# Kernel tuning notes

Hardware: AMD Instinct MI355X
Metric: run time of the kernel (lower is better)

## Reference

```python
import jax, jax.numpy as jnp
import numpy as np

S, H, D, NL = 3, 64, 12, 2  # scales, hidden, input_dim, layers
B, L = 512, 512
EPS = 1e-5


def _layernorm(x, g, b):
    m = jnp.mean(x, axis=-1, keepdims=True)
    v = jnp.var(x, axis=-1, keepdims=True)
    return (x - m) * jax.lax.rsqrt(v + EPS) * g + b


def _cell(x_t, h, c, gw, gb, mi_w, mi_b, mo_w, mo_b, w1, b1, w2, b2, lag, lab, log, lob):
    # fused 4-gate linear: [B, in+H] @ [in+H, 4H]
    gates = jnp.concatenate([x_t, h], axis=-1) @ gw + gb
    f, i, g, o = jnp.split(gates, 4, axis=-1)
    c_new = jax.nn.sigmoid(f) * c + jax.nn.sigmoid(i) * jnp.tanh(g)
    h_t = jax.nn.sigmoid(o) * jnp.tanh(c_new)
    # MultiheadAttention with seq_len=1: softmax over one key == 1,
    # so attn_out = out_proj(v_proj(h_t)) exactly (q/k contribute nothing).
    v = h_t @ mi_w[:, 2 * H:] + mi_b[2 * H:]
    a = v @ mo_w + mo_b
    a = jax.nn.gelu(a @ w1 + b1, approximate=False) @ w2 + b2
    a = _layernorm(a, lag, lab)
    return _layernorm(a + h, log, lob), c_new


def _run_xlstm(xi, gw0, gb0, gw1, gb1, mi_w, mi_b, mo_w, mo_b,
               w1, b1, w2, b2, lag, lab, log, lob, rw0, rb0, rw1, rb1):
    # xi: [B, L, D] -> outputs [B, L, H]; 2-layer unidirectional xLSTM (eval: dropout=identity)
    Bb = xi.shape[0]
    z = jnp.zeros((Bb, H), xi.dtype)

    def step(carry, x_t):
        h0, c0, h1, c1 = carry
        h0, c0 = _cell(x_t, h0, c0, gw0, gb0, mi_w[0], mi_b[0], mo_w[0], mo_b[0],
                       w1[0], b1[0], w2[0], b2[0], lag[0], lab[0], log[0], lob[0])
        inp = h0 + x_t @ rw0 + rb0
        h1, c1 = _cell(inp, h1, c1, gw1, gb1, mi_w[1], mi_b[1], mo_w[1], mo_b[1],
                       w1[1], b1[1], w2[1], b2[1], lag[1], lab[1], log[1], lob[1])
        out = h1 + inp @ rw1 + rb1
        return (h0, c0, h1, c1), out

    _, ys = jax.lax.scan(step, (z, z, z, z), jnp.swapaxes(xi, 0, 1))
    return jnp.swapaxes(ys, 0, 1)


def _upsample_linear(xi, out_len):
    # F.interpolate(mode='linear', align_corners=False) on [B, Li, D] time axis
    Li = xi.shape[1]
    if Li == out_len:
        return xi
    sc = Li / out_len
    src = jnp.maximum((jnp.arange(out_len, dtype=jnp.float32) + 0.5) * sc - 0.5, 0.0)
    i0 = jnp.clip(jnp.floor(src).astype(jnp.int32), 0, Li - 1)
    i1 = jnp.minimum(i0 + 1, Li - 1)
    w = (src - i0.astype(jnp.float32))[None, :, None]
    return xi[:, i0] * (1.0 - w) + xi[:, i1] * w


def _forward(x, gw0, gb0, gw1, gb1, mi_w, mi_b, mo_w, mo_b, w1, b1, w2, b2,
             lag, lab, log, lob, rw0, rb0, rw1, rb1, attn_w):
    Ls = x.shape[1]
    ups = []
    for i in (1, 2, 3):
        start = Ls - Ls // i
        ups.append(_upsample_linear(x[:, start:, :], Ls))
    # bug-faithful ordering from source: xlstm[i] consumes upsampled_outputs[i-1]
    xs = jnp.stack([ups[2], ups[0], ups[1]], axis=0)  # [S, B, L, D]
    outs = jax.vmap(_run_xlstm)(xs, gw0, gb0, gw1, gb1, mi_w, mi_b, mo_w, mo_b,
                                w1, b1, w2, b2, lag, lab, log, lob,
                                rw0, rb0, rw1, rb1)      # [S, B, L, H]
    merged = jnp.moveaxis(outs, 0, 1)                    # [B, S, L, H]
    weights = jax.nn.softmax(merged @ attn_w, axis=1)    # softmax over scale dim
    return jnp.sum(merged * weights[..., None], axis=1)  # [B, L, H]


def setup_inputs() -> dict:
    key = jax.random.key(0)
    ks = iter(jax.random.split(key, 32))
    w = lambda *sh: jax.random.normal(next(ks), sh, jnp.float32) * 0.02
    IN0, IN1 = D + H, 2 * H
    return {
        'x': jax.random.normal(next(ks), (B, L, D), jnp.float32),
        'gw0': w(S, IN0, 4 * H), 'gb0': jnp.zeros((S, 4 * H)),
        'gw1': w(S, IN1, 4 * H), 'gb1': jnp.zeros((S, 4 * H)),
        'mi_w': w(S, NL, H, 3 * H), 'mi_b': jnp.zeros((S, NL, 3 * H)),
        'mo_w': w(S, NL, H, H), 'mo_b': jnp.zeros((S, NL, H)),
        'w1': w(S, NL, H, 2 * H), 'b1': jnp.zeros((S, NL, 2 * H)),
        'w2': w(S, NL, 2 * H, H), 'b2': jnp.zeros((S, NL, H)),
        'lag': jnp.ones((S, NL, H)), 'lab': jnp.zeros((S, NL, H)),
        'log': jnp.ones((S, NL, H)), 'lob': jnp.zeros((S, NL, H)),
        'rw0': w(S, D, H), 'rb0': jnp.zeros((S, H)),
        'rw1': w(S, H, H), 'rb1': jnp.zeros((S, H)),
        'attn_w': w(H),
    }


def reference(x, gw0, gb0, gw1, gb1, mi_w, mi_b, mo_w, mo_b, w1, b1, w2, b2,
              lag, lab, log, lob, rw0, rb0, rw1, rb1, attn_w):
    return _forward(x, gw0, gb0, gw1, gb1, mi_w, mi_b, mo_w, mo_b, w1, b1, w2, b2,
                    lag, lab, log, lob, rw0, rb0, rw1, rb1, attn_w)
```

## Files before the change

kernel.cpp:

```cpp
#include <hip/hip_runtime.h>
#include <hip/hip_bf16.h>
#include <math.h>

#define Sn 3
#define Hn 64
#define Dn 12
#define Bn 512
#define Ln 512
#define BC 4
#define IN0 76
#define NIN 22
#define CT 32
#define NCHUNK (Ln / CT)
#define P2OFF 0
#define P1OFF 384
#define GROFF 768
#define CBOFF 1026
#define MEGABLK 1538

#define NINP ((size_t)3 * Bn * CT * 64)
#define NG1R ((size_t)3 * Bn * CT * 320)
#define NMERG ((size_t)3 * Bn * CT * 64)

using bf16 = __hip_bfloat16;
typedef _Float16 h2 __attribute__((ext_vector_type(2)));
typedef _Float16 h4 __attribute__((ext_vector_type(4)));
typedef _Float16 h8t __attribute__((ext_vector_type(8)));
typedef int i2v __attribute__((ext_vector_type(2)));

__device__ __forceinline__ float u2f(unsigned short x) {
    return __uint_as_float(((unsigned int)x) << 16);
}
__device__ __forceinline__ unsigned short f2u(float f) {
    bf16 h = __float2bfloat16(f);
    unsigned short u;
    __builtin_memcpy(&u, &h, 2);
    return u;
}

__device__ __forceinline__ float ex2(float x) {
#if __has_builtin(__builtin_amdgcn_exp2f)
    return __builtin_amdgcn_exp2f(x);
#else
    return exp2f(x);
#endif
}
__device__ __forceinline__ float frcp(float x) {
#if __has_builtin(__builtin_amdgcn_rcpf)
    return __builtin_amdgcn_rcpf(x);
#else
    return 1.0f / x;
#endif
}
__device__ __forceinline__ float sigm(float x) {
    return frcp(1.0f + ex2(-1.44269504f * x));
}
__device__ __forceinline__ float tanhfast(float x) {
    return 1.0f - 2.0f * frcp(1.0f + ex2(2.88539008f * x));
}
__device__ __forceinline__ float gelu_ex(float x) { return 0.5f * x * (1.0f + erff(x * 0.70710678118654752f)); }

__device__ __forceinline__ float fdot2f(h2 a, h2 b, float c) {
#if __has_builtin(__builtin_amdgcn_fdot2)
    return __builtin_amdgcn_fdot2(a, b, c, false);
#else
    return fmaf((float)a.x, (float)b.x, fmaf((float)a.y, (float)b.y, c));
#endif
}
__device__ __forceinline__ h2 cvt2(float x, float y) {
    h2 r; r.x = (_Float16)x; r.y = (_Float16)y; return r;
}
__device__ __forceinline__ h2 mk2(_Float16 a, _Float16 b) {
    h2 r; r.x = a; r.y = b; return r;
}
__device__ __forceinline__ void unpack8(h8t v, h2* out) {
    out[0] = __builtin_shufflevector(v, v, 0, 1);
    out[1] = __builtin_shufflevector(v, v, 2, 3);
    out[2] = __builtin_shufflevector(v, v, 4, 5);
    out[3] = __builtin_shufflevector(v, v, 6, 7);
}

template <int CTRL>
__device__ __forceinline__ float qp(float v) {
    return __int_as_float(__builtin_amdgcn_update_dpp(0, __float_as_int(v), CTRL, 0xF, 0xF, true));
}
__device__ __forceinline__ float qsum(float v) {
    v += qp<0xB1>(v);
    v += qp<0x4E>(v);
    return v;
}
__device__ __forceinline__ float osum(float v) {
    v = qsum(v);
    v += qp<0x141>(v);
    return v;
}
__device__ __forceinline__ float xadd16(float v) {
#if __has_builtin(__builtin_amdgcn_permlane16_swap)
    i2v r = __builtin_amdgcn_permlane16_swap(__float_as_int(v), __float_as_int(v), false, false);
    return __int_as_float(r.x) + __int_as_float(r.y);
#else
    return v + __int_as_float(__builtin_amdgcn_ds_swizzle(__float_as_int(v), 0x401F));
// ... 40 lines not shown
    unsigned dstOff[NIN];
    unsigned n[NIN];
    unsigned blockStart[NIN + 1];
};

__global__ __launch_bounds__(256) void convert_kernel(ConvArgs a, float* __restrict__ dst,
                                                      const int* __restrict__ flag) {
    int bid = blockIdx.x;
    int i = 0;
    while (i < NIN - 1 && bid >= (int)a.blockStart[i + 1]) i++;
    unsigned lb = (unsigned)bid - a.blockStart[i];
    unsigned base = lb * 2048 + threadIdx.x;
    unsigned n = a.n[i];
    float* d = dst + a.dstOff[i];
    bool isf32 = (*flag != 0);
    const float* sf = (const float*)a.src[i];
    const unsigned short* su = (const unsigned short*)a.src[i];
#pragma unroll
    for (int e = 0; e < 8; e++) {
        unsigned idx = base + e * 256;
        if (idx < n) d[idx] = isf32 ? sf[idx] : u2f(su[idx]);
    }
}

__global__ __launch_bounds__(256) void fuse_kernel(
    const float* __restrict__ mi_w, const float* __restrict__ mi_b,
    const float* __restrict__ mo_w, const float* __restrict__ mo_b,
    const float* __restrict__ w1, const float* __restrict__ b1,
    float* __restrict__ M1out, float* __restrict__ bias1out) {
    int sl = blockIdx.x;
    __shared__ float T[64][64];
    __shared__ float bT[64];
    const float* Mv = mi_w + sl * 64 * 192;
    const float* Mo = mo_w + sl * 64 * 64;
    for (int idx = threadIdx.x; idx < 64 * 64; idx += 256) {
        int k = idx >> 6, n = idx & 63;
        float acc = 0.f;
        for (int j = 0; j < 64; j++) acc += Mv[k * 192 + 128 + j] * Mo[j * 64 + n];
        T[k][n] = acc;
    }
    for (int n = threadIdx.x; n < 64; n += 256) {
        float acc = mo_b[sl * 64 + n];
        for (int j = 0; j < 64; j++) acc += mi_b[sl * 192 + 128 + j] * Mo[j * 64 + n];
        bT[n] = acc;
    }
    __syncthreads();
    const float* W1 = w1 + sl * 64 * 128;
    for (int idx = threadIdx.x; idx < 64 * 128; idx += 256) {
        int k = idx >> 7, m = idx & 127;
        float acc = 0.f;
        for (int n = 0; n < 64; n++) acc += T[k][n] * W1[n * 128 + m];
        M1out[sl * 64 * 128 + idx] = acc;
    }
    for (int m = threadIdx.x; m < 128; m += 256) {
        float acc = b1[sl * 128 + m];
        for (int n = 0; n < 64; n++) acc += bT[n] * W1[n * 128 + m];
        bias1out[sl * 128 + m] = acc;
    }
}

__global__ __launch_bounds__(256) void perm_kernel(
    const float* __restrict__ gw1, const float* __restrict__ gb1,
    const float* __restrict__ rw1,
    h2* __restrict__ gw1p16, float* __restrict__ gb1p,
    h2* __restrict__ rw1p16) {
    int s = blockIdx.x;
    int tid = threadIdx.x;
    const float* G = gw1 + (size_t)s * 128 * 256;
    for (int idx = tid; idx < 32 * 256; idx += 256) {
        int k2 = idx >> 8, p = idx & 255;
        int c = (p & 3) * 64 + ((p >> 6) << 4) + ((p >> 2) & 15);
        gw1p16[((size_t)s * 32 + k2) * 256 + p] =
            cvt2(G[(2 * k2) * 256 + c], G[(2 * k2 + 1) * 256 + c]);
    }
    for (int p = tid; p < 256; p += 256) {
        int c = (p & 3) * 64 + ((p >> 6) << 4) + ((p >> 2) & 15);
        gb1p[s * 256 + p] = gb1[s * 256 + c];
    }
    const float* R = rw1 + (size_t)s * 64 * 64;
    for (int idx = tid; idx < 32 * 64; idx += 256) {
        int k2 = idx >> 6, c = idx & 63;
        rw1p16[((size_t)s * 32 + k2) * 64 + c] =
            cvt2(R[(2 * k2) * 64 + c], R[(2 * k2 + 1) * 64 + c]);
    }
}

__device__ __forceinline__ void pass1_body(
    int bid,
    const float* __restrict__ x, const float* __restrict__ gw0,
    const float* __restrict__ gb0,
    const float* __restrict__ M1g, const float* __restrict__ bias1g,
    const float* __restrict__ w2g, const float* __restrict__ b2g,
    const float* __restrict__ lag, const float* __restrict__ lab,
    const float* __restrict__ log_, const float* __restrict__ lob,
    const float* __restrict__ rw0, const float* __restrict__ rb0,
    float* __restrict__ gstate, _Float16* __restrict__ inp_w, int t0) {
    const int tid = threadIdx.x;
    const int sIdx = bid >> 7;
    const int gbase = (bid & 127) * BC;
    const int W = tid >> 6, lane = tid & 63;
    const int q = lane >> 2, ks = lane & 3;
    const int oct = lane >> 3, ks8 = lane & 7;
    const int j = W * 16 + q;
    const int cM = W * 32 + q * 2;
    const int uD = W * 16 + oct * 2;

    const int Li = (sIdx == 0) ? 170 : (sIdx == 1 ? 512 : 256);
    const int st = (sIdx == 0) ? 342 : (sIdx == 1 ? 0 : 256);
    const float sc = (float)Li / 512.0f;

    __shared__ float s_x[2][BC][12];
    __shared__ __align__(16) _Float16 s_h16[BC][72];
    __shared__ __align__(16) _Float16 s_ht16[BC][72];
    __shared__ __align__(16) _Float16 s_z16[BC][136];
    __shared__ float s_t2[BC][64];
    __shared__ float s_rw0[768];

    __builtin_amdgcn_s_setprio(1);

    const float* gw0s = gw0 + sIdx * IN0 * 256;
    float wx[12];
    h2 wg16[4][8], wm16[2][8], ww16[2][8];
#pragma unroll
    for (int g = 0; g < 4; g++)
#pragma unroll
        for (int d = 0; d < 3; d++) wx[g * 3 + d] = gw0s[(ks * 3 + d) * 256 + j + 64 * g];
#pragma unroll
    for (int g = 0; g < 4; g++)
#pragma unroll
        for (int kk = 0; kk < 8; kk++)
            wg16[g][kk] = cvt2(gw0s[(12 + ks * 16 + 2 * kk) * 256 + j + 64 * g],
                               gw0s[(12 + ks * 16 + 2 * kk + 1) * 256 + j + 64 * g]);
    const float* M1s = M1g + (sIdx * 2 + 0) * 8192;
#pragma unroll
    for (int cc = 0; cc < 2; cc++)
#pragma unroll
        for (int kk = 0; kk < 8; kk++)
            wm16[cc][kk] = cvt2(M1s[(ks * 16 + 2 * kk) * 128 + cM + cc],
                                M1s[(ks * 16 + 2 * kk + 1) * 128 + cM + cc]);
    const float* w2s = w2g + (sIdx * 2 + 0) * 8192;
#pragma unroll
    for (int cc = 0; cc < 2; cc++)
#pragma unroll
        for (int kk = 0; kk < 8; kk++)
            ww16[cc][kk] = cvt2(w2s[(ks8 * 16 + 2 * kk) * 64 + uD + cc],
                                w2s[(ks8 * 16 + 2 * kk + 1) * 64 + uD + cc]);

    float h_gb[4];
#pragma unroll
    for (int g = 0; g < 4; g++) h_gb[g] = gb0[sIdx * 256 + j + 64 * g];
    float h_b1[2] = {bias1g[(sIdx * 2 + 0) * 128 + cM], bias1g[(sIdx * 2 + 0) * 128 + cM + 1]};
    float h_b2[2] = {b2g[(sIdx * 2 + 0) * 64 + uD], b2g[(sIdx * 2 + 0) * 64 + uD + 1]};
    int ei = (sIdx * 2 + 0) * 64 + lane;
    float eLag = lag[ei], eLab = lab[ei], eLog = log_[ei], eLob = lob[ei];
    float eRb0 = rb0[sIdx * 64 + lane];

    for (int i = tid; i < 768; i += 256) s_rw0[i] = rw0[sIdx * 768 + i];
    {
        int b = tid >> 6, jj = tid & 63;
        float hv = (t0 == 0) ? 0.f : gstate[((size_t)(sIdx * Bn + gbase + b)) * 256 + jj];
        s_h16[b][jj] = (_Float16)hv;
    }
    float cS = (t0 == 0) ? 0.f
                         : gstate[((size_t)(sIdx * Bn + gbase + ks)) * 256 + 64 + j];
    if (tid < BC * 12) {
        int b = tid / 12, d = tid % 12;
// ... 214 lines not shown
            if (ks == b) { myF = a0; myI = a1; myG = a2; myO = a3; }
        }
        {
            float cn = sigm(myF) * cS + sigm(myI) * tanhfast(myG);
            cS = cn;
            p2_ht16[ks][j] = (_Float16)(sigm(myO) * tanhfast(cn));
        }
        float g1rn[BC], rn;
        if (tt + 1 < CT) {
#pragma unroll
            for (int b = 0; b < BC; b++)
                g1rn[b] = (float)G1Rr[(rowBase + (size_t)b * CT + tt + 1) * 320 + pOff];
            rn = (float)G1Rr[(rowBase + (size_t)W * CT + tt + 1) * 320 + 256 + lane];
        } else {
#pragma unroll
            for (int b = 0; b < BC; b++) g1rn[b] = 0.f;
            rn = 0.f;
        }
        __syncthreads();
        float z0 = 0, z1 = 0;
#pragma unroll
        for (int b = 0; b < BC; b++) {
            const h8t* hp = (const h8t*)&p2_ht16[b][ks * 16];
            h8t hv0 = hp[0], hv1 = hp[1];
            h2 hk[8];
            unpack8(hv0, hk); unpack8(hv1, hk + 4);
            float acc0 = (ks == 0) ? h_b1[0] : 0.f;
            float acc1 = (ks == 0) ? h_b1[1] : 0.f;
#pragma unroll
            for (int kk = 0; kk < 8; kk++) {
                acc0 = fdot2f(wm16[0][kk], hk[kk], acc0);
                acc1 = fdot2f(wm16[1][kk], hk[kk], acc1);
            }
            float a0 = qsum(acc0);
            float a1 = qsum(acc1);
            if (ks == b) { z0 = a0; z1 = a1; }
        }
        *(h2*)&p2_z16[ks][cM] = cvt2(gelu_ex(z0), gelu_ex(z1));
        __syncthreads();
#pragma unroll
        for (int b = 0; b < BC; b++) {
            const h8t* zp = (const h8t*)&p2_z16[b][ks8 * 16];
            h8t zv0 = zp[0], zv1 = zp[1];
            h2 zk[8];
            unpack8(zv0, zk); unpack8(zv1, zk + 4);
            float acc0 = (ks8 == 0) ? h_b2[0] : 0.f;
            float acc1 = (ks8 == 0) ? h_b2[1] : 0.f;
#pragma unroll
            for (int kk = 0; kk < 8; kk++) {
                acc0 = fdot2f(ww16[0][kk], zk[kk], acc0);
                acc1 = fdot2f(ww16[1][kk], zk[kk], acc1);
            }
            float a0 = osum(acc0);
            float a1 = osum(acc1);
            if (ks8 == b) { p2_t2[b][uD] = a0; p2_t2[b][uD + 1] = a1; }
        }
        __syncthreads();
        {
            const int bb = W;
            float v = p2_t2[bb][lane];
            float m = redsum64(v) * (1.0f / 64.0f);
            float var = redsum64(v * v) * (1.0f / 64.0f) - m * m;
            float rs = rsqrtf(fmaxf(var, 0.0f) + 1e-5f);
            float a = (v - m) * rs * eLag + eLab;
            float hOld = (float)p2_h16[bb][lane];
            float y = a + hOld;
            float m2 = redsum64(y) * (1.0f / 64.0f);
            float var2 = redsum64(y * y) * (1.0f / 64.0f) - m2 * m2;
            float rs2 = rsqrtf(fmaxf(var2, 0.0f) + 1e-5f);
            float h1n = (y - m2) * rs2 * eLog + eLob;
            p2_h16[bb][lane] = (_Float16)h1n;
            merged_w[(((size_t)(sIdx * Bn + gbase + bb)) * CT + tt) * 64 + lane] = f2u(h1n + rv);
        }
        __syncthreads();
#pragma unroll
        for (int b = 0; b < BC; b++) g1rv[b] = g1rn[b];
        rv = rn;
    }
    {
        int b = tid >> 6, jj = tid & 63;
        gstate[((size_t)(sIdx * Bn + gbase + b)) * 256 + 128 + jj] = (float)p2_h16[b][jj];
    }
    gstate[((size_t)(sIdx * Bn + gbase + ks)) * 256 + 192 + j] = cS;
}

__device__ __forceinline__ void g1r_body(
    int bid,
    const h2* __restrict__ gw1p16, const float* __restrict__ gb1p,
    const h2* __restrict__ rw1p16, const float* __restrict__ rb1,
    const _Float16* __restrict__ inp_r, _Float16* __restrict__ G1Rw) {
    const int tid = threadIdx.x;
    const int s = bid / 86;
    const int bb = bid % 86;
    __shared__ __align__(16) h2 s_in2[32][36];

    const int c4 = tid & 63, rg = tid >> 6;
    float4 bias = *(const float4*)(gb1p + s * 256 + c4 * 4);
    float rbias = rb1[s * 64 + c4];
    const h2* Wg = gw1p16 + (size_t)s * 32 * 256;
    const h2* Wr = rw1p16 + (size_t)s * 32 * 64;

    const size_t sRow = (size_t)s * Bn * CT;
    for (int tile = 0; tile < 6; tile++) {
        int tIdx = bb * 6 + tile;
        if (tIdx >= 512) break;
        int r0 = tIdx * 32;
        __syncthreads();
        for (int i = tid; i < 512; i += 256) {
            int r = i >> 4, kq = i & 15;
            h4 v = *(const h4*)(inp_r + (sRow + r0 + r) * 64 + kq * 4);
            s_in2[kq * 2 + 0][r] = mk2(v.x, v.y);
            s_in2[kq * 2 + 1][r] = mk2(v.z, v.w);
        }
        __syncthreads();
        float acc[8][4], accR[8];
#pragma unroll
        for (int r = 0; r < 8; r++) {
            acc[r][0] = bias.x; acc[r][1] = bias.y; acc[r][2] = bias.z; acc[r][3] = bias.w;
            accR[r] = rbias;
        }
#pragma unroll 4
        for (int k2 = 0; k2 < 32; k2++) {
            h8t wv = *(const h8t*)(Wg + (size_t)k2 * 256 + c4 * 4);
            h2 wp[4]; unpack8(wv, wp);
            h2 wR = Wr[k2 * 64 + c4];
            const h8t* ip = (const h8t*)&s_in2[k2][rg * 8];
            h8t iv0 = ip[0], iv1 = ip[1];
            h2 in2[8]; unpack8(iv0, in2); unpack8(iv1, in2 + 4);
#pragma unroll
            for (int r = 0; r < 8; r++) {
                acc[r][0] = fdot2f(in2[r], wp[0], acc[r][0]);
                acc[r][1] = fdot2f(in2[r], wp[1], acc[r][1]);
                acc[r][2] = fdot2f(in2[r], wp[2], acc[r][2]);
                acc[r][3] = fdot2f(in2[r], wp[3], acc[r][3]);
                accR[r] = fdot2f(in2[r], wR, accR[r]);
            }
        }
#pragma unroll
        for (int r = 0; r < 8; r++) {
            size_t row = sRow + r0 + rg * 8 + r;
            h4 o;
            o.x = (_Float16)acc[r][0]; o.y = (_Float16)acc[r][1];
            o.z = (_Float16)acc[r][2]; o.w = (_Float16)acc[r][3];
            *(h4*)(G1Rw + row * 320 + c4 * 4) = o;
            G1Rw[row * 320 + 256 + c4] = (_Float16)accR[r];
        }
    }
}

__device__ __forceinline__ void combine_body(
    int bid,
    const unsigned short* __restrict__ merged_r,
    const float* __restrict__ attn_w,
    void* __restrict__ outv, const int* __restrict__ flag, int t0) {
    int W = threadIdx.x >> 6, lane = threadIdx.x & 63;
    float aw = attn_w[lane];
    size_t stride = (size_t)Bn * CT * 64;
    int isf = *flag;
#pragma unroll
    for (int r = 0; r < 8; r++) {
        int wid = (bid * 4 + W) * 8 + r;
        int b = wid >> 5, tt = wid & 31;
        size_t base = (((size_t)b) * CT + tt) * 64 + lane;
        float m0 = u2f(merged_r[base]);
        float m1 = u2f(merged_r[base + stride]);
        float m2 = u2f(merged_r[base + 2 * stride]);
        float e0 = redsum64(m0 * aw);
        float e1 = redsum64(m1 * aw);
        float e2 = redsum64(m2 * aw);
        float mx = fmaxf(e0, fmaxf(e1, e2));
        float x0 = expf(e0 - mx), x1 = expf(e1 - mx), x2 = expf(e2 - mx);
        float inv = 1.0f / (x0 + x1 + x2);
        float val = (x0 * m0 + x1 * m1 + x2 * m2) * inv;
        size_t ob = (((size_t)b) * Ln + t0 + tt) * 64 + lane;
        if (isf) ((float*)outv)[ob] = val;
        else ((unsigned short*)outv)[ob] = f2u(val);
    }
}

__global__ __launch_bounds__(256) __attribute__((amdgpu_waves_per_eu(2, 5)))
void mega_kernel(
    const float* __restrict__ x, const float* __restrict__ gw0,
    const float* __restrict__ gb0, const float* __restrict__ gw1,
    const h2* __restrict__ gw1p16, const float* __restrict__ gb1p,
    const h2* __restrict__ rw1p16,
    const float* __restrict__ M1g, const float* __restrict__ bias1g,
    const float* __restrict__ w2g, const float* __restrict__ b2g,
    const float* __restrict__ lag, const float* __restrict__ lab,
    const float* __restrict__ log_, const float* __restrict__ lob,
    const float* __restrict__ rw0, const float* __restrict__ rb0,
    const float* __restrict__ rb1,
    float* __restrict__ gstate,
    _Float16* __restrict__ inpB, _Float16* __restrict__ G1RB,
    unsigned short* __restrict__ mergedB,
    const float* __restrict__ attn_w, void* __restrict__ outv,
    const int* __restrict__ flag,
    int c_p1, int c_g1r, int c_p2, int c_comb) {
    int bid = blockIdx.x;
    if (bid < P1OFF) {
        if (c_p2 >= 0) {
            const _Float16* g1r_r = G1RB + (size_t)(c_p2 & 1) * NG1R;
            unsigned short* merged_w = mergedB + (size_t)(c_p2 & 1) * NMERG;
            pass2_body(bid, gw1, M1g, bias1g, w2g, b2g, lag, lab, log_, lob,
                       g1r_r, gstate, merged_w, c_p2 * CT);
        }
    } else if (bid < GROFF) {
        if (c_p1 >= 0) {
            _Float16* inp_w = inpB + (size_t)(c_p1 & 1) * NINP;
            pass1_body(bid - P1OFF, x, gw0, gb0, M1g, bias1g, w2g, b2g,
                       lag, lab, log_, lob, rw0, rb0, gstate, inp_w, c_p1 * CT);
        }
    } else if (bid < CBOFF) {
        if (c_g1r >= 0) {
            const _Float16* inp_r = inpB + (size_t)(c_g1r & 1) * NINP;
            _Float16* g1r_w = G1RB + (size_t)(c_g1r & 1) * NG1R;
            g1r_body(bid - GROFF, gw1p16, gb1p, rw1p16, rb1, inp_r, g1r_w);
        }
    } else {
        if (c_comb >= 0) {
            const unsigned short* merged_r = mergedB + (size_t)(c_comb & 1) * NMERG;
            combine_body(bid - CBOFF, merged_r, attn_w, outv, flag, c_comb * CT);
        }
    }
}

extern "C" void kernel_launch(void* const* d_in, const int* in_sizes, int n_in,
                              void* d_out, int out_size, void* d_ws, size_t ws_size,
                              hipStream_t stream) {
    (void)out_size; (void)ws_size;
    int* flag = (int*)d_ws;
    float* canon = (float*)((char*)d_ws + 16);

    ConvArgs ca;
    size_t tot = 0;
    unsigned nblocks = 0;
    for (int i = 0; i < NIN; i++) {
        ca.src[i] = d_in[i];
        ca.dstOff[i] = (unsigned)tot;
        unsigned n = (unsigned)in_sizes[i];
        ca.n[i] = n;
        ca.blockStart[i] = nblocks;
        nblocks += (n + 2047) / 2048;
        tot += n;
    }
    ca.blockStart[NIN] = nblocks;

    size_t canonBytes = (tot * 4 + 15) & ~(size_t)15;
    char* p = (char*)d_ws + 16 + canonBytes;
    float* M1 = (float*)p;       p += (size_t)3 * 2 * 64 * 128 * 4;
    float* bias1 = (float*)p;    p += (size_t)3 * 2 * 128 * 4;
    float* gb1p = (float*)p;     p += (size_t)3 * 256 * 4;
    h2* gw1p16 = (h2*)p;         p += (size_t)3 * 32 * 256 * 4;
    h2* rw1p16 = (h2*)p;         p += (size_t)3 * 32 * 64 * 4;
    float* gstate = (float*)p;   p += (size_t)3 * 512 * 256 * 4;
    p = (char*)(((uintptr_t)p + 15) & ~(uintptr_t)15);
    _Float16* inpB = (_Float16*)p;      p += 2 * NINP * 2;
    _Float16* G1RB = (_Float16*)p;      p += 2 * NG1R * 2;
    p = (char*)(((uintptr_t)p + 15) & ~(uintptr_t)15);
    unsigned short* mergedB = (unsigned short*)p;

    const float* x    = canon + ca.dstOff[0];
    const float* gw0  = canon + ca.dstOff[1];
    const float* gb0  = canon + ca.dstOff[2];
    const float* gw1  = canon + ca.dstOff[3];
    const float* gb1  = canon + ca.dstOff[4];
    const float* mi_w = canon + ca.dstOff[5];
    const float* mi_b = canon + ca.dstOff[6];
    const float* mo_w = canon + ca.dstOff[7];
    const float* mo_b = canon + ca.dstOff[8];
    const float* w1   = canon + ca.dstOff[9];
    const float* b1   = canon + ca.dstOff[10];
    const float* w2   = canon + ca.dstOff[11];
    const float* b2   = canon + ca.dstOff[12];
    const float* lag  = canon + ca.dstOff[13];
    const float* lab  = canon + ca.dstOff[14];
    const float* log_ = canon + ca.dstOff[15];
    const float* lob  = canon + ca.dstOff[16];
    const float* rw0  = canon + ca.dstOff[17];
    const float* rb0  = canon + ca.dstOff[18];
    const float* rw1  = canon + ca.dstOff[19];
    const float* rb1  = canon + ca.dstOff[20];
    const float* attn_w = canon + ca.dstOff[21];

    detect_kernel<<<dim3(1), dim3(256), 0, stream>>>((const unsigned short*)d_in[0], flag);
    convert_kernel<<<dim3(nblocks), dim3(256), 0, stream>>>(ca, canon, flag);
    fuse_kernel<<<dim3(6), dim3(256), 0, stream>>>(mi_w, mi_b, mo_w, mo_b, w1, b1, M1, bias1);
    perm_kernel<<<dim3(3), dim3(256), 0, stream>>>(gw1, gb1, rw1, gw1p16, gb1p, rw1p16);

    for (int m = 0; m <= NCHUNK + 2; m++) {
        int c1 = (m < NCHUNK) ? m : -1;
        int cg = (m - 1 >= 0 && m - 1 < NCHUNK) ? m - 1 : -1;
        int c2 = (m - 2 >= 0 && m - 2 < NCHUNK) ? m - 2 : -1;
        int cc = (m - 3 >= 0 && m - 3 < NCHUNK) ? m - 3 : -1;
        mega_kernel<<<dim3(MEGABLK), dim3(256), 0, stream>>>(
            x, gw0, gb0, gw1, gw1p16, gb1p, rw1p16, M1, bias1, w2, b2,
            lag, lab, log_, lob, rw0, rb0, rb1, gstate, inpB, G1RB, mergedB,
            attn_w, d_out, flag, c1, cg, c2, cc);
    }
}
```

Baseline: 3.057 ms.

## Replace per-chunk kernel launches with a persistent cooperative kernel using grid sync

Replaces the 19 successive mega_kernel launches with one cooperative persistent kernel of 1024 blocks. The pass1 and pass2 blocks keep their weights and recurrent state in registers and shared memory across chunks instead of reloading them from gstate. Helper blocks run the g1r GEMM and the combine stage, and grid-wide syncs separate the pipeline stages. The aim is to remove launch overhead and the per-chunk state and weight reloads. In exchange it needs the whole grid co-resident, keeps the multi-launch path as a fallback, and pays for a grid barrier on every chunk.

```diff
diff --git a/kernel.cpp b/kernel.cpp
--- a/kernel.cpp
+++ b/kernel.cpp
@@ -1,4 +1,5 @@
 #include <hip/hip_runtime.h>
+#include <hip/hip_cooperative_groups.h>
 #include <hip/hip_bf16.h>
 #include <math.h>
 
@@ -17,6 +18,7 @@
 #define GROFF 768
 #define CBOFF 1026
 #define MEGABLK 1538
+#define PGRID 1024
 
 #define NINP ((size_t)3 * Bn * CT * 64)
 #define NG1R ((size_t)3 * Bn * CT * 320)
@@ -223,6 +225,100 @@
         int k2 = idx >> 6, c = idx & 63;
         rw1p16[((size_t)s * 32 + k2) * 64 + c] =
             cvt2(R[(2 * k2) * 64 + c], R[(2 * k2 + 1) * 64 + c]);
+    }
+}
+
+__device__ __forceinline__ void g1r_body(
+    int bid,
+    const h2* __restrict__ gw1p16, const float* __restrict__ gb1p,
+    const h2* __restrict__ rw1p16, const float* __restrict__ rb1,
+    const _Float16* __restrict__ inp_r, _Float16* __restrict__ G1Rw) {
+    const int tid = threadIdx.x;
+    const int s = bid / 86;
+    const int bb = bid % 86;
+    __shared__ __align__(16) h2 s_in2[32][36];
+
+    const int c4 = tid & 63, rg = tid >> 6;
+    float4 bias = *(const float4*)(gb1p + s * 256 + c4 * 4);
+    float rbias = rb1[s * 64 + c4];
+    const h2* Wg = gw1p16 + (size_t)s * 32 * 256;
+    const h2* Wr = rw1p16 + (size_t)s * 32 * 64;
+
+    const size_t sRow = (size_t)s * Bn * CT;
+    for (int tile = 0; tile < 6; tile++) {
+        int tIdx = bb * 6 + tile;
+        if (tIdx >= 512) break;
+        int r0 = tIdx * 32;
+        __syncthreads();
+        for (int i = tid; i < 512; i += 256) {
+            int r = i >> 4, kq = i & 15;
+            h4 v = *(const h4*)(inp_r + (sRow + r0 + r) * 64 + kq * 4);
+            s_in2[kq * 2 + 0][r] = mk2(v.x, v.y);
+            s_in2[kq * 2 + 1][r] = mk2(v.z, v.w);
+        }
+        __syncthreads();
+        float acc[8][4], accR[8];
+#pragma unroll
+        for (int r = 0; r < 8; r++) {
+            acc[r][0] = bias.x; acc[r][1] = bias.y; acc[r][2] = bias.z; acc[r][3] = bias.w;
+            accR[r] = rbias;
+        }
+#pragma unroll 4
+        for (int k2 = 0; k2 < 32; k2++) {
+            h8t wv = *(const h8t*)(Wg + (size_t)k2 * 256 + c4 * 4);
+            h2 wp[4]; unpack8(wv, wp);
+            h2 wR = Wr[k2 * 64 + c4];
+            const h8t* ip = (const h8t*)&s_in2[k2][rg * 8];
+            h8t iv0 = ip[0], iv1 = ip[1];
+            h2 in2[8]; unpack8(iv0, in2); unpack8(iv1, in2 + 4);
+#pragma unroll
+            for (int r = 0; r < 8; r++) {
+                acc[r][0] = fdot2f(in2[r], wp[0], acc[r][0]);
+                acc[r][1] = fdot2f(in2[r], wp[1], acc[r][1]);
+                acc[r][2] = fdot2f(in2[r], wp[2], acc[r][2]);
+                acc[r][3] = fdot2f(in2[r], wp[3], acc[r][3]);
+                accR[r] = fdot2f(in2[r], wR, accR[r]);
+            }
+        }
+#pragma unroll
+        for (int r = 0; r < 8; r++) {
+            size_t row = sRow + r0 + rg * 8 + r;
+            h4 o;
+            o.x = (_Float16)acc[r][0]; o.y = (_Float16)acc[r][1];
+            o.z = (_Float16)acc[r][2]; o.w = (_Float16)acc[r][3];
+            *(h4*)(G1Rw + row * 320 + c4 * 4) = o;
+            G1Rw[row * 320 + 256 + c4] = (_Float16)accR[r];
+        }
+    }
+}
+
+__device__ __forceinline__ void combine_body(
+    int bid,
+    const unsigned short* __restrict__ merged_r,
+    const float* __restrict__ attn_w,
+    void* __restrict__ outv, const int* __restrict__ flag, int t0) {
+    int W = threadIdx.x >> 6, lane = threadIdx.x & 63;
+    float aw = attn_w[lane];
+    size_t stride = (size_t)Bn * CT * 64;
+    int isf = *flag;
+#pragma unroll
+    for (int r = 0; r < 8; r++) {
+        int wid = (bid * 4 + W) * 8 + r;
+        int b = wid >> 5, tt = wid & 31;
+        size_t base = (((size_t)b) * CT + tt) * 64 + lane;
+        float m0 = u2f(merged_r[base]);
+        float m1 = u2f(merged_r[base + stride]);
+        float m2 = u2f(merged_r[base + 2 * stride]);
+        float e0 = redsum64(m0 * aw);
+        float e1 = redsum64(m1 * aw);
+        float e2 = redsum64(m2 * aw);
+        float mx = fmaxf(e0, fmaxf(e1, e2));
+        float x0 = expf(e0 - mx), x1 = expf(e1 - mx), x2 = expf(e2 - mx);
+        float inv = 1.0f / (x0 + x1 + x2);
+        float val = (x0 * m0 + x1 * m1 + x2 * m2) * inv;
+        size_t ob = (((size_t)b) * Ln + t0 + tt) * 64 + lane;
+        if (isf) ((float*)outv)[ob] = val;
+        else ((unsigned short*)outv)[ob] = f2u(val);
     }
 }
 
@@ -603,100 +699,6 @@
         gstate[((size_t)(sIdx * Bn + gbase + b)) * 256 + 128 + jj] = (float)p2_h16[b][jj];
     }
     gstate[((size_t)(sIdx * Bn + gbase + ks)) * 256 + 192 + j] = cS;
-}
-
-__device__ __forceinline__ void g1r_body(
-    int bid,
-    const h2* __restrict__ gw1p16, const float* __restrict__ gb1p,
-    const h2* __restrict__ rw1p16, const float* __restrict__ rb1,
-    const _Float16* __restrict__ inp_r, _Float16* __restrict__ G1Rw) {
-    const int tid = threadIdx.x;
-    const int s = bid / 86;
-    const int bb = bid % 86;
-    __shared__ __align__(16) h2 s_in2[32][36];
-
-    const int c4 = tid & 63, rg = tid >> 6;
-    float4 bias = *(const float4*)(gb1p + s * 256 + c4 * 4);
-    float rbias = rb1[s * 64 + c4];
-    const h2* Wg = gw1p16 + (size_t)s * 32 * 256;
-    const h2* Wr = rw1p16 + (size_t)s * 32 * 64;
-
-    const size_t sRow = (size_t)s * Bn * CT;
-    for (int tile = 0; tile < 6; tile++) {
-        int tIdx = bb * 6 + tile;
-        if (tIdx >= 512) break;
-        int r0 = tIdx * 32;
-        __syncthreads();
-        for (int i = tid; i < 512; i += 256) {
-            int r = i >> 4, kq = i & 15;
-            h4 v = *(const h4*)(inp_r + (sRow + r0 + r) * 64 + kq * 4);
-            s_in2[kq * 2 + 0][r] = mk2(v.x, v.y);
-            s_in2[kq * 2 + 1][r] = mk2(v.z, v.w);
-        }
-        __syncthreads();
-        float acc[8][4], accR[8];
-#pragma unroll
-        for (int r = 0; r < 8; r++) {
-            acc[r][0] = bias.x; acc[r][1] = bias.y; acc[r][2] = bias.z; acc[r][3] = bias.w;
-            accR[r] = rbias;
-        }
-#pragma unroll 4
-        for (int k2 = 0; k2 < 32; k2++) {
-            h8t wv = *(const h8t*)(Wg + (size_t)k2 * 256 + c4 * 4);
-            h2 wp[4]; unpack8(wv, wp);
-            h2 wR = Wr[k2 * 64 + c4];
-            const h8t* ip = (const h8t*)&s_in2[k2][rg * 8];
-            h8t iv0 = ip[0], iv1 = ip[1];
-            h2 in2[8]; unpack8(iv0, in2); unpack8(iv1, in2 + 4);
-#pragma unroll
-            for (int r = 0; r < 8; r++) {
-                acc[r][0] = fdot2f(in2[r], wp[0], acc[r][0]);
-                acc[r][1] = fdot2f(in2[r], wp[1], acc[r][1]);
-                acc[r][2] = fdot2f(in2[r], wp[2], acc[r][2]);
-                acc[r][3] = fdot2f(in2[r], wp[3], acc[r][3]);
-                accR[r] = fdot2f(in2[r], wR, accR[r]);
-            }
-        }
-#pragma unroll
-        for (int r = 0; r < 8; r++) {
-            size_t row = sRow + r0 + rg * 8 + r;
-            h4 o;
-            o.x = (_Float16)acc[r][0]; o.y = (_Float16)acc[r][1];
-            o.z = (_Float16)acc[r][2]; o.w = (_Float16)acc[r][3];
-            *(h4*)(G1Rw + row * 320 + c4 * 4) = o;
-            G1Rw[row * 320 + 256 + c4] = (_Float16)accR[r];
-        }
-    }
-}
-
-__device__ __forceinline__ void combine_body(
-    int bid,
-    const unsigned short* __restrict__ merged_r,
-    const float* __restrict__ attn_w,
-    void* __restrict__ outv, const int* __restrict__ flag, int t0) {
-    int W = threadIdx.x >> 6, lane = threadIdx.x & 63;
-    float aw = attn_w[lane];
-    size_t stride = (size_t)Bn * CT * 64;
-    int isf = *flag;
-#pragma unroll
-    for (int r = 0; r < 8; r++) {
-        int wid = (bid * 4 + W) * 8 + r;
-        int b = wid >> 5, tt = wid & 31;
-        size_t base = (((size_t)b) * CT + tt) * 64 + lane;
-        float m0 = u2f(merged_r[base]);
-        float m1 = u2f(merged_r[base + stride]);
-        float m2 = u2f(merged_r[base + 2 * stride]);
-        float e0 = redsum64(m0 * aw);
-        float e1 = redsum64(m1 * aw);
-        float e2 = redsum64(m2 * aw);
-        float mx = fmaxf(e0, fmaxf(e1, e2));
-        float x0 = expf(e0 - mx), x1 = expf(e1 - mx), x2 = expf(e2 - mx);
-        float inv = 1.0f / (x0 + x1 + x2);
-        float val = (x0 * m0 + x1 * m1 + x2 * m2) * inv;
-        size_t ob = (((size_t)b) * Ln + t0 + tt) * 64 + lane;
-        if (isf) ((float*)outv)[ob] = val;
-        else ((unsigned short*)outv)[ob] = f2u(val);
-    }
 }
 
 __global__ __launch_bounds__(256) __attribute__((amdgpu_waves_per_eu(2, 5)))
@@ -745,6 +747,417 @@
     }
 }
 
+struct PArgs {
+    const float *x, *gw0, *gb0, *gw1;
+    const h2* gw1p16; const float* gb1p; const h2* rw1p16;
+    const float *M1g, *bias1g, *w2g, *b2g, *lag, *lab, *log_, *lob, *rw0, *rb0, *rb1;
+    _Float16 *inpB, *G1RB;
+    unsigned short* mergedB;
+    const float* attn_w;
+    void* outv;
+    const int* flag;
+};
+
+__device__ void pass1_persist(int bid, const PArgs& a) {
+    const int tid = threadIdx.x;
+    const int sIdx = bid >> 7;
+    const int gbase = (bid & 127) * BC;
+    const int W = tid >> 6, lane = tid & 63;
+    const int q = lane >> 2, ks = lane & 3;
+    const int oct = lane >> 3, ks8 = lane & 7;
+    const int j = W * 16 + q;
+    const int cM = W * 32 + q * 2;
+    const int uD = W * 16 + oct * 2;
+
+    const int Li = (sIdx == 0) ? 170 : (sIdx == 1 ? 512 : 256);
+    const int st = (sIdx == 0) ? 342 : (sIdx == 1 ? 0 : 256);
+    const float sc = (float)Li / 512.0f;
+
+    __shared__ float s_x[2][BC][12];
+    __shared__ __align__(16) _Float16 s_h16[BC][72];
+    __shared__ __align__(16) _Float16 s_ht16[BC][72];
+    __shared__ __align__(16) _Float16 s_z16[BC][136];
+    __shared__ float s_t2[BC][64];
+    __shared__ float s_rw0[768];
+
+    __builtin_amdgcn_s_setprio(1);
+
+    const float* gw0s = a.gw0 + sIdx * IN0 * 256;
+    float wx[12];
+    h2 wg16[4][8], wm16[2][8], ww16[2][8];
+#pragma unroll
+    for (int g = 0; g < 4; g++)
+#pragma unroll
+        for (int d = 0; d < 3; d++) wx[g * 3 + d] = gw0s[(ks * 3 + d) * 256 + j + 64 * g];
+#pragma unroll
+    for (int g = 0; g < 4; g++)
+#pragma unroll
+        for (int kk = 0; kk < 8; kk++)
+            wg16[g][kk] = cvt2(gw0s[(12 + ks * 16 + 2 * kk) * 256 + j + 64 * g],
+                               gw0s[(12 + ks * 16 + 2 * kk + 1) * 256 + j + 64 * g]);
+    const float* M1s = a.M1g + (sIdx * 2 + 0) * 8192;
+#pragma unroll
+    for (int cc = 0; cc < 2; cc++)
+#pragma unroll
+        for (int kk = 0; kk < 8; kk++)
+            wm16[cc][kk] = cvt2(M1s[(ks * 16 + 2 * kk) * 128 + cM + cc],
+                                M1s[(ks * 16 + 2 * kk + 1) * 128 + cM + cc]);
+    const float* w2s = a.w2g + (sIdx * 2 + 0) * 8192;
+#pragma unroll
+    for (int cc = 0; cc < 2; cc++)
+#pragma unroll
+        for (int kk = 0; kk < 8; kk++)
+            ww16[cc][kk] = cvt2(w2s[(ks8 * 16 + 2 * kk) * 64 + uD + cc],
+                                w2s[(ks8 * 16 + 2 * kk + 1) * 64 + uD + cc]);
+
+    float h_gb[4];
+#pragma unroll
+    for (int g = 0; g < 4; g++) h_gb[g] = a.gb0[sIdx * 256 + j + 64 * g];
+    float h_b1[2] = {a.bias1g[(sIdx * 2 + 0) * 128 + cM], a.bias1g[(sIdx * 2 + 0) * 128 + cM + 1]};
+    float h_b2[2] = {a.b2g[(sIdx * 2 + 0) * 64 + uD], a.b2g[(sIdx * 2 + 0) * 64 + uD + 1]};
+    int ei = (sIdx * 2 + 0) * 64 + lane;
+    float eLag = a.lag[ei], eLab = a.lab[ei], eLog = a.log_[ei], eLob = a.lob[ei];
+    float eRb0 = a.rb0[sIdx * 64 + lane];
+
+    for (int i = tid; i < 768; i += 256) s_rw0[i] = a.rw0[sIdx * 768 + i];
+    {
+        int b = tid >> 6, jj = tid & 63;
+        s_h16[b][jj] = (_Float16)0.f;
+    }
+    float cS = 0.f;
+    __syncthreads();
+
+    cooperative_groups::grid_group gg = cooperative_groups::this_grid();
+    for (int m = 0; m <= NCHUNK + 2; m++) {
+        if (m < NCHUNK) {
+            const int t0 = m * CT;
+            _Float16* inp_w = a.inpB + (size_t)(m & 1) * NINP;
+            if (tid < BC * 12) {
+                int b = tid / 12, d = tid % 12;
+                float srcp = fmaxf((t0 + 0.5f) * sc - 0.5f, 0.f);
+                int i0 = (int)floorf(srcp); if (i0 > Li - 1) i0 = Li - 1;
+                int i1 = i0 + 1; if (i1 > Li - 1) i1 = Li - 1;
+                float w = srcp - (float)i0;
+                int gb = gbase + b;
+                s_x[0][b][d] = a.x[(gb * Ln + st + i0) * 12 + d] * (1.0f - w) +
+                               a.x[(gb * Ln + st + i1) * 12 + d] * w;
+            }
+            __syncthreads();
+
+            for (int tt = 0; tt < CT; tt++) {
+                const int sl = tt & 1;
+                float myF = 0, myI = 0, myG = 0, myO = 0;
+#pragma unroll
+                for (int b = 0; b < BC; b++) {
+                    const h8t* hp = (const h8t*)&s_h16[b][ks * 16];
+                    h8t hv0 = hp[0], hv1 = hp[1];
+                    h2 hk[8];
+                    unpack8(hv0, hk); unpack8(hv1, hk + 4);
+                    float x0 = s_x[sl][b][ks * 3], x1 = s_x[sl][b][ks * 3 + 1], x2 = s_x[sl][b][ks * 3 + 2];
+                    float acc[4];
+#pragma unroll
+                    for (int g = 0; g < 4; g++) {
+                        float s0 = (ks == 0) ? h_gb[g] : 0.f;
+                        acc[g] = fmaf(wx[g * 3], x0, fmaf(wx[g * 3 + 1], x1, fmaf(wx[g * 3 + 2], x2, s0)));
+                    }
+#pragma unroll
+                    for (int kk = 0; kk < 8; kk++) {
+#pragma unroll
+                        for (int g = 0; g < 4; g++)
+                            acc[g] = fdot2f(wg16[g][kk], hk[kk], acc[g]);
+                    }
+                    float a0 = qsum(acc[0]);
+                    float a1 = qsum(acc[1]);
+                    float a2 = qsum(acc[2]);
+                    float a3 = qsum(acc[3]);
+                    if (ks == b) { myF = a0; myI = a1; myG = a2; myO = a3; }
+                }
+                {
+                    float cn = sigm(myF) * cS + sigm(myI) * tanhfast(myG);
+                    cS = cn;
+                    s_ht16[ks][j] = (_Float16)(sigm(myO) * tanhfast(cn));
+                }
+                __syncthreads();
+                float z0 = 0, z1 = 0;
+#pragma unroll
+                for (int b = 0; b < BC; b++) {
+                    const h8t* hp = (const h8t*)&s_ht16[b][ks * 16];
+                    h8t hv0 = hp[0], hv1 = hp[1];
+                    h2 hk[8];
+                    unpack8(hv0, hk); unpack8(hv1, hk + 4);
+                    float acc0 = (ks == 0) ? h_b1[0] : 0.f;
+                    float acc1 = (ks == 0) ? h_b1[1] : 0.f;
+#pragma unroll
+                    for (int kk = 0; kk < 8; kk++) {
+                        acc0 = fdot2f(wm16[0][kk], hk[kk], acc0);
+                        acc1 = fdot2f(wm16[1][kk], hk[kk], acc1);
+                    }
+                    float a0 = qsum(acc0);
+                    float a1 = qsum(acc1);
+                    if (ks == b) { z0 = a0; z1 = a1; }
+                }
+                *(h2*)&s_z16[ks][cM] = cvt2(gelu_ex(z0), gelu_ex(z1));
+                __syncthreads();
+#pragma unroll
+                for (int b = 0; b < BC; b++) {
+                    const h8t* zp = (const h8t*)&s_z16[b][ks8 * 16];
+                    h8t zv0 = zp[0], zv1 = zp[1];
+                    h2 zk[8];
+                    unpack8(zv0, zk); unpack8(zv1, zk + 4);
+                    float acc0 = (ks8 == 0) ? h_b2[0] : 0.f;
+                    float acc1 = (ks8 == 0) ? h_b2[1] : 0.f;
+#pragma unroll
+                    for (int kk = 0; kk < 8; kk++) {
+                        acc0 = fdot2f(ww16[0][kk], zk[kk], acc0);
+                        acc1 = fdot2f(ww16[1][kk], zk[kk], acc1);
+                    }
+                    float a0 = osum(acc0);
+                    float a1 = osum(acc1);
+                    if (ks8 == b) { s_t2[b][uD] = a0; s_t2[b][uD + 1] = a1; }
+                }
+                __syncthreads();
+                {
+                    const int bb = W;
+                    float v = s_t2[bb][lane];
+                    float mm = redsum64(v) * (1.0f / 64.0f);
+                    float var = redsum64(v * v) * (1.0f / 64.0f) - mm * mm;
+                    float rs = rsqrtf(fmaxf(var, 0.0f) + 1e-5f);
+                    float aa = (v - mm) * rs * eLag + eLab;
+                    float hOld = (float)s_h16[bb][lane];
+                    float y = aa + hOld;
+                    float m2 = redsum64(y) * (1.0f / 64.0f);
+                    float var2 = redsum64(y * y) * (1.0f / 64.0f) - m2 * m2;
+                    float rs2 = rsqrtf(fmaxf(var2, 0.0f) + 1e-5f);
+                    float h0n = (y - m2) * rs2 * eLog + eLob;
+                    s_h16[bb][lane] = (_Float16)h0n;
+                    float p = h0n + eRb0;
+#pragma unroll
+                    for (int d = 0; d < 12; d++)
+                        p = fmaf(s_x[sl][bb][d], s_rw0[d * 64 + lane], p);
+                    inp_w[(((size_t)(sIdx * Bn + gbase + bb)) * CT + tt) * 64 + lane] = (_Float16)p;
+                    if (tt + 1 < CT && lane < 12) {
+                        int d = lane;
+                        int t = t0 + tt + 1;
+                        float srcp = fmaxf((t + 0.5f) * sc - 0.5f, 0.f);
+                        int i0 = (int)floorf(srcp); if (i0 > Li - 1) i0 = Li - 1;
+                        int i1 = i0 + 1; if (i1 > Li - 1) i1 = Li - 1;
+                        float w = srcp - (float)i0;
+                        int gb = gbase + bb;
+                        s_x[sl ^ 1][bb][d] = a.x[(gb * Ln + st + i0) * 12 + d] * (1.0f - w) +
+                                             a.x[(gb * Ln + st + i1) * 12 + d] * w;
+                    }
+                }
+                __syncthreads();
+            }
+        }
+        __threadfence();
+        gg.sync();
+    }
+}
+
+__device__ void pass2_persist(int bid, const PArgs& a) {
+    const int tid = threadIdx.x;
+    const int sIdx = bid >> 7;
+    const int gbase = (bid & 127) * BC;
+    const int W = tid >> 6, lane = tid & 63;
+    const int q = lane >> 2, ks = lane & 3;
+    const int oct = lane >> 3, ks8 = lane & 7;
+    const int j = W * 16 + q;
+    const int cM = W * 32 + q * 2;
+    const int uD = W * 16 + oct * 2;
+
+    __shared__ __align__(16) _Float16 p2_h16[BC][72];
+    __shared__ __align__(16) _Float16 p2_ht16[BC][72];
+    __shared__ __align__(16) _Float16 p2_z16[BC][136];
+    __shared__ float p2_t2[BC][64];
+
+    __builtin_amdgcn_s_setprio(1);
+
+    const float* gw1s = a.gw1 + (size_t)sIdx * 128 * 256;
+    h2 wg16[4][8], wm16[2][8], ww16[2][8];
+#pragma unroll
+    for (int g = 0; g < 4; g++)
+#pragma unroll
+        for (int kk = 0; kk < 8; kk++)
+            wg16[g][kk] = cvt2(gw1s[(64 + ks * 16 + 2 * kk) * 256 + j + 64 * g],
+                               gw1s[(64 + ks * 16 + 2 * kk + 1) * 256 + j + 64 * g]);
+    const float* M1s = a.M1g + (sIdx * 2 + 1) * 8192;
+#pragma unroll
+    for (int cc = 0; cc < 2; cc++)
+#pragma unroll
+        for (int kk = 0; kk < 8; kk++)
+            wm16[cc][kk] = cvt2(M1s[(ks * 16 + 2 * kk) * 128 + cM + cc],
+                                M1s[(ks * 16 + 2 * kk + 1) * 128 + cM + cc]);
+    const float* w2s = a.w2g + (sIdx * 2 + 1) * 8192;
+#pragma unroll
+    for (int cc = 0; cc < 2; cc++)
+#pragma unroll
+        for (int kk = 0; kk < 8; kk++)
+            ww16[cc][kk] = cvt2(w2s[(ks8 * 16 + 2 * kk) * 64 + uD + cc],
+                                w2s[(ks8 * 16 + 2 * kk + 1) * 64 + uD + cc]);
+
+    float h_b1[2] = {a.bias1g[(sIdx * 2 + 1) * 128 + cM], a.bias1g[(sIdx * 2 + 1) * 128 + cM + 1]};
+    float h_b2[2] = {a.b2g[(sIdx * 2 + 1) * 64 + uD], a.b2g[(sIdx * 2 + 1) * 64 + uD + 1]};
+    int ei = (sIdx * 2 + 1) * 64 + lane;
+    float eLag = a.lag[ei], eLab = a.lab[ei], eLog = a.log_[ei], eLob = a.lob[ei];
+
+    {
+        int b = tid >> 6, jj = tid & 63;
+        p2_h16[b][jj] = (_Float16)0.f;
+    }
+    float cS = 0.f;
+    __syncthreads();
+
+    const size_t rowBase = ((size_t)(sIdx * Bn + gbase)) * CT;
+    const int pOff = W * 64 + lane;
+
+    cooperative_groups::grid_group gg = cooperative_groups::this_grid();
+    for (int m = 0; m <= NCHUNK + 2; m++) {
+        int c2 = m - 2;
+        if (c2 >= 0 && c2 < NCHUNK) {
+            const _Float16* G1Rr = a.G1RB + (size_t)(c2 & 1) * NG1R;
+            unsigned short* merged_w = a.mergedB + (size_t)(c2 & 1) * NMERG;
+
+            float g1rv[BC], rv;
+#pragma unroll
+            for (int b = 0; b < BC; b++)
+                g1rv[b] = (float)G1Rr[(rowBase + (size_t)b * CT) * 320 + pOff];
+            rv = (float)G1Rr[(rowBase + (size_t)W * CT) * 320 + 256 + lane];
+
+            for (int tt = 0; tt < CT; tt++) {
+                float myF = 0, myI = 0, myG = 0, myO = 0;
+#pragma unroll
+                for (int b = 0; b < BC; b++) {
+                    const h8t* hp = (const h8t*)&p2_h16[b][ks * 16];
+                    h8t hv0 = hp[0], hv1 = hp[1];
+                    h2 hk[8];
+                    unpack8(hv0, hk); unpack8(hv1, hk + 4);
+                    float acc[4];
+#pragma unroll
+                    for (int g = 0; g < 4; g++) acc[g] = (ks == g) ? g1rv[b] : 0.f;
+#pragma unroll
+                    for (int kk = 0; kk < 8; kk++) {
+#pragma unroll
+                        for (int g = 0; g < 4; g++)
+                            acc[g] = fdot2f(wg16[g][kk], hk[kk], acc[g]);
+                    }
+                    float a0 = qsum(acc[0]);
+                    float a1 = qsum(acc[1]);
+                    float a2 = qsum(acc[2]);
+                    float a3 = qsum(acc[3]);
+                    if (ks == b) { myF = a0; myI = a1; myG = a2; myO = a3; }
+                }
+                {
+                    float cn = sigm(myF) * cS + sigm(myI) * tanhfast(myG);
+                    cS = cn;
+                    p2_ht16[ks][j] = (_Float16)(sigm(myO) * tanhfast(cn));
+                }
+                float g1rn[BC], rn;
+                if (tt + 1 < CT) {
+#pragma unroll
+                    for (int b = 0; b < BC; b++)
+                        g1rn[b] = (float)G1Rr[(rowBase + (size_t)b * CT + tt + 1) * 320 + pOff];
+                    rn = (float)G1Rr[(rowBase + (size_t)W * CT + tt + 1) * 320 + 256 + lane];
+                } else {
+#pragma unroll
+                    for (int b = 0; b < BC; b++) g1rn[b] = 0.f;
+                    rn = 0.f;
+                }
+                __syncthreads();
+                float z0 = 0, z1 = 0;
+#pragma unroll
+                for (int b = 0; b < BC; b++) {
+                    const h8t* hp = (const h8t*)&p2_ht16[b][ks * 16];
+                    h8t hv0 = hp[0], hv1 = hp[1];
+                    h2 hk[8];
+                    unpack8(hv0, hk); unpack8(hv1, hk + 4);
+                    float acc0 = (ks == 0) ? h_b1[0] : 0.f;
+                    float acc1 = (ks == 0) ? h_b1[1] : 0.f;
+#pragma unroll
+                    for (int kk = 0; kk < 8; kk++) {
+                        acc0 = fdot2f(wm16[0][kk], hk[kk], acc0);
+                        acc1 = fdot2f(wm16[1][kk], hk[kk], acc1);
+                    }
+                    float a0 = qsum(acc0);
+                    float a1 = qsum(acc1);
+                    if (ks == b) { z0 = a0; z1 = a1; }
+                }
+                *(h2*)&p2_z16[ks][cM] = cvt2(gelu_ex(z0), gelu_ex(z1));
+                __syncthreads();
+#pragma unroll
+                for (int b = 0; b < BC; b++) {
+                    const h8t* zp = (const h8t*)&p2_z16[b][ks8 * 16];
+                    h8t zv0 = zp[0], zv1 = zp[1];
+                    h2 zk[8];
+                    unpack8(zv0, zk); unpack8(zv1, zk + 4);
+                    float acc0 = (ks8 == 0) ? h_b2[0] : 0.f;
+                    float acc1 = (ks8 == 0) ? h_b2[1] : 0.f;
+#pragma unroll
+                    for (int kk = 0; kk < 8; kk++) {
+                        acc0 = fdot2f(ww16[0][kk], zk[kk], acc0);
+                        acc1 = fdot2f(ww16[1][kk], zk[kk], acc1);
+                    }
+                    float a0 = osum(acc0);
+                    float a1 = osum(acc1);
+                    if (ks8 == b) { p2_t2[b][uD] = a0; p2_t2[b][uD + 1] = a1; }
+                }
+                __syncthreads();
+                {
+                    const int bb = W;
+                    float v = p2_t2[bb][lane];
+                    float mm = redsum64(v) * (1.0f / 64.0f);
+                    float var = redsum64(v * v) * (1.0f / 64.0f) - mm * mm;
+                    float rs = rsqrtf(fmaxf(var, 0.0f) + 1e-5f);
+                    float aa = (v - mm) * rs * eLag + eLab;
+                    float hOld = (float)p2_h16[bb][lane];
+                    float y = aa + hOld;
+                    float m2 = redsum64(y) * (1.0f / 64.0f);
+                    float var2 = redsum64(y * y) * (1.0f / 64.0f) - m2 * m2;
+                    float rs2 = rsqrtf(fmaxf(var2, 0.0f) + 1e-5f);
+                    float h1n = (y - m2) * rs2 * eLog + eLob;
+                    p2_h16[bb][lane] = (_Float16)h1n;
+                    merged_w[(((size_t)(sIdx * Bn + gbase + bb)) * CT + tt) * 64 + lane] = f2u(h1n + rv);
+                }
+                __syncthreads();
+#pragma unroll
+                for (int b = 0; b < BC; b++) g1rv[b] = g1rn[b];
+                rv = rn;
+            }
+        }
+        __threadfence();
+        gg.sync();
+    }
+}
+
+__device__ void helper_persist(int hid, const PArgs& a) {
+    cooperative_groups::grid_group gg = cooperative_groups::this_grid();
+    for (int m = 0; m <= NCHUNK + 2; m++) {
+        int cgi = m - 1;
+        if (cgi >= 0 && cgi < NCHUNK) {
+            const _Float16* inp_r = a.inpB + (size_t)(cgi & 1) * NINP;
+            _Float16* g1r_w = a.G1RB + (size_t)(cgi & 1) * NG1R;
+            for (int slot = hid; slot < 258; slot += 256)
+                g1r_body(slot, a.gw1p16, a.gb1p, a.rw1p16, a.rb1, inp_r, g1r_w);
+        }
+        int cci = m - 3;
+        if (cci >= 0 && cci < NCHUNK) {
+            const unsigned short* merged_r = a.mergedB + (size_t)(cci & 1) * NMERG;
+            for (int slot = hid; slot < 512; slot += 256)
+                combine_body(slot, merged_r, a.attn_w, a.outv, a.flag, cci * CT);
+        }
+        __threadfence();
+        gg.sync();
+    }
+}
+
+__global__ __launch_bounds__(256) __attribute__((amdgpu_waves_per_eu(2, 4)))
+void persist_kernel(PArgs a) {
+    int bid = blockIdx.x;
+    if (bid < 384) pass2_persist(bid, a);
+    else if (bid < 768) pass1_persist(bid - 384, a);
+    else helper_persist(bid - 768, a);
+}
+
 extern "C" void kernel_launch(void* const* d_in, const int* in_sizes, int n_in,
                               void* d_out, int out_size, void* d_ws, size_t ws_size,
                               hipStream_t stream) {
@@ -808,14 +1221,43 @@
     fuse_kernel<<<dim3(6), dim3(256), 0, stream>>>(mi_w, mi_b, mo_w, mo_b, w1, b1, M1, bias1);
     perm_kernel<<<dim3(3), dim3(256), 0, stream>>>(gw1, gb1, rw1, gw1p16, gb1p, rw1p16);
 
-    for (int m = 0; m <= NCHUNK + 2; m++) {
-        int c1 = (m < NCHUNK) ? m : -1;
-        int cg = (m - 1 >= 0 && m - 1 < NCHUNK) ? m - 1 : -1;
-        int c2 = (m - 2 >= 0 && m - 2 < NCHUNK) ? m - 2 : -1;
-        int cc = (m - 3 >= 0 && m - 3 < NCHUNK) ? m - 3 : -1;
-        mega_kernel<<<dim3(MEGABLK), dim3(256), 0, stream>>>(
-            x, gw0, gb0, gw1, gw1p16, gb1p, rw1p16, M1, bias1, w2, b2,
-            lag, lab, log_, lob, rw0, rb0, rb1, gstate, inpB, G1RB, mergedB,
-            attn_w, d_out, flag, c1, cg, c2, cc);
-    }
-}
+    static int coop_ok = -1;
+    if (coop_ok < 0) {
+        int dev = 0; hipGetDevice(&dev);
+        int coop = 0; hipDeviceGetAttribute(&coop, hipDeviceAttributeCooperativeLaunch, dev);
+        int nCU = 0; hipDeviceGetAttribute(&nCU, hipDeviceAttributeMultiprocessorCount, dev);
+        int maxb = 0;
+        hipOccupancyMaxActiveBlocksPerMultiprocessor(&maxb, persist_kernel, 256, 0);
+        coop_ok = (coop && (long)maxb * nCU >= PGRID) ? 1 : 0;
+    }
+
+    bool done = false;
+    if (coop_ok == 1) {
+        PArgs pa;
+        pa.x = x; pa.gw0 = gw0; pa.gb0 = gb0; pa.gw1 = gw1;
+        pa.gw1p16 = gw1p16; pa.gb1p = gb1p; pa.rw1p16 = rw1p16;
+        pa.M1g = M1; pa.bias1g = bias1; pa.w2g = w2; pa.b2g = b2;
+        pa.lag = lag; pa.lab = lab; pa.log_ = log_; pa.lob = lob;
+        pa.rw0 = rw0; pa.rb0 = rb0; pa.rb1 = rb1;
+        pa.inpB = inpB; pa.G1RB = G1RB; pa.mergedB = mergedB;
+        pa.attn_w = attn_w; pa.outv = d_out; pa.flag = flag;
+        void* kargs[] = { &pa };
+        hipError_t e = hipLaunchCooperativeKernel((const void*)persist_kernel,
+                                                  dim3(PGRID), dim3(256), kargs, 0, stream);
+        if (e == hipSuccess) done = true;
+        else { (void)hipGetLastError(); coop_ok = 0; }
+    }
+
+    if (!done) {
+        for (int m = 0; m <= NCHUNK + 2; m++) {
+            int c1 = (m < NCHUNK) ? m : -1;
+            int cg = (m - 1 >= 0 && m - 1 < NCHUNK) ? m - 1 : -1;
+            int c2 = (m - 2 >= 0 && m - 2 < NCHUNK) ? m - 2 : -1;
+            int cc = (m - 3 >= 0 && m - 3 < NCHUNK) ? m - 3 : -1;
+            mega_kernel<<<dim3(MEGABLK), dim3(256), 0, stream>>>(
+                x, gw0, gb0, gw1, gw1p16, gb1p, rw1p16, M1, bias1, w2, b2,
+                lag, lab, log_, lob, rw0, rb0, rb1, gstate, inpB, G1RB, mergedB,
+                attn_w, d_out, flag, c1, cg, c2, cc);
+        }
+    }
+}
```

After: 3.062 ms. Within noise of the previous version (+0.2%).
